# Kernel optimization log

Hardware: AMD Instinct MI355X
Metric: run time of the kernel (lower is better)

The kernel has to match this reference:

```python
import jax, jax.numpy as jnp
import numpy as np

EPS = 1e-6  # matches the ~1e-6 diagonal jitter added in tensor_log


def _make_spd(key, shape_bm, d):
    a = jax.random.normal(key, shape_bm + (d, d), dtype=jnp.float32)
    x = jnp.einsum('bmik,bmjk->bmij', a, a) / d
    return x + 0.1 * jnp.eye(d, dtype=jnp.float32)


def _make_stiefel(key, out_dim, in_dim):
    a = jax.random.normal(key, (in_dim, out_dim), dtype=jnp.float32)
    q, _ = jnp.linalg.qr(a)  # (in_dim, out_dim), orthonormal columns
    return q.T  # (out_dim, in_dim), semi-orthogonal rows


def setup_inputs() -> dict:
    key = jax.random.key(0)
    ks = jax.random.split(key, 8)
    bs, m, din, dqk, dv = 32, 64, 96, 48, 48
    return {
        'x1': _make_spd(ks[0], (bs, m), din),
        'x2': _make_spd(ks[1], (bs, m), din),
        'wq1': _make_stiefel(ks[2], dqk, din),
        'wk1': _make_stiefel(ks[3], dqk, din),
        'wv1': _make_stiefel(ks[4], dv, din),
        'wq2': _make_stiefel(ks[5], dqk, din),
        'wk2': _make_stiefel(ks[6], dqk, din),
        'wv2': _make_stiefel(ks[7], dv, din),
    }


def _logm(t):
    # symmetric matrix log via eigh (inputs SPD); tiny diag jitter as in torch tensor_log
    d = t.shape[-1]
    t = t + EPS * jnp.eye(d, dtype=t.dtype)
    s, u = jnp.linalg.eigh(t)
    return jnp.einsum('...ik,...k,...jk->...ij', u, jnp.log(s), u)


def _expm(t):
    s, u = jnp.linalg.eigh(t)
    return jnp.einsum('...ik,...k,...jk->...ij', u, jnp.exp(s), u)


def _bimap(x, w):
    # SPDTransform: W X W^T, W: (out, in), x: [..., in, in]
    return jnp.einsum('oi,...ij,pj->...op', w, x, w)


def reference(x1, x2, wq1, wk1, wv1, wq2, wk2, wv2):
    # per-stream q/k/v BiMap transforms, then concat along token axis
    Q = jnp.concatenate([_bimap(x1, wq1), _bimap(x2, wq2)], axis=1)  # [b, m, dqk, dqk]
    K = jnp.concatenate([_bimap(x1, wk1), _bimap(x2, wk2)], axis=1)
    V = jnp.concatenate([_bimap(x1, wv1), _bimap(x2, wv2)], axis=1)  # [b, m, dv, dv]

    logQ, logK, logV = _logm(Q), _logm(K), _logm(V)

    # log-Euclidean distance: sum of singular values of D D^T = ||D||_F^2,
    # D = logQ_j - logK_i. energy[b, i, j] matches torch repeat/expand layout
    q2 = jnp.sum(logQ * logQ, axis=(-2, -1))  # [b, m]
    k2 = jnp.sum(logK * logK, axis=(-2, -1))  # [b, m]
    cross = jnp.einsum('bjxy,bixy->bij', logQ, logK)  # [b, i(K), j(Q)]
    energy = q2[:, None, :] + k2[:, :, None] - 2.0 * cross
    energy = jnp.maximum(energy, 0.0)

    scores = 1.0 / (1.0 + jnp.log1p(energy))
    prob = jax.nn.softmax(scores, axis=-2)  # softmax over K index
    prob = jnp.transpose(prob, (0, 2, 1))   # [b, j, i]

    bs, m, dv, _ = V.shape
    mixed = (prob @ logV.reshape(bs, m, dv * dv)).reshape(bs, m, dv, dv)
    out = _expm(mixed)
    out = out[:, -1:, :, :]  # keep_only_last=True
    return out.reshape(-1, dv, dv)  # [bs, dv, dv]
```

## Files before the change

kernel.cpp:

```cpp
#include <hip/hip_runtime.h>
#include <math.h>

#define D_CHEB 24

typedef __attribute__((ext_vector_type(8))) short bf16x8;
typedef __attribute__((ext_vector_type(4))) short bf16x4;
typedef __attribute__((ext_vector_type(4))) float f32x4;
typedef __attribute__((ext_vector_type(4))) unsigned int u32x4;
typedef __attribute__((ext_vector_type(2))) unsigned int u32x2;

#if __has_builtin(__builtin_amdgcn_mfma_f32_16x16x16bf16_1k)
#define HAVE_MFMA16 1
#else
#define HAVE_MFMA16 0
#endif

struct Cheb {
    float c[D_CHEB + 1];
    float sm;
    float sbd;
};

__device__ __forceinline__ void split8(const f32x4 a, const f32x4 b,
                                       bf16x8& hi, bf16x8& lo)
{
    float v[8] = {a[0], a[1], a[2], a[3], b[0], b[1], b[2], b[3]};
    unsigned h16[8], l16[8];
    #pragma unroll
    for (int j = 0; j < 8; ++j) {
        unsigned u = __float_as_uint(v[j]);
        unsigned r = (u + 0x7FFFu + ((u >> 16) & 1u)) >> 16;
        h16[j] = r;
        float res = v[j] - __uint_as_float(r << 16);
        l16[j] = __float_as_uint(res) >> 16;
    }
    unsigned hw[4], lw[4];
    #pragma unroll
    for (int q = 0; q < 4; ++q) {
        hw[q] = h16[2 * q] | (h16[2 * q + 1] << 16);
        lw[q] = l16[2 * q] | (l16[2 * q + 1] << 16);
    }
    hi = __builtin_bit_cast(bf16x8, (u32x4){hw[0], hw[1], hw[2], hw[3]});
    lo = __builtin_bit_cast(bf16x8, (u32x4){lw[0], lw[1], lw[2], lw[3]});
}

__global__ __launch_bounds__(256) void split_w(
    const float* __restrict__ w0, const float* __restrict__ w1,
    const float* __restrict__ w2, const float* __restrict__ w3,
    const float* __restrict__ w4,
    unsigned short* __restrict__ whi, unsigned short* __restrict__ wlo)
{
    const float* W = (blockIdx.x == 0) ? w0 : (blockIdx.x == 1) ? w1
                   : (blockIdx.x == 2) ? w2 : (blockIdx.x == 3) ? w3 : w4;
    const int base = blockIdx.x * 4608;
    for (int e = threadIdx.x; e < 4608; e += 256) {
        float f = W[e];
        unsigned u = __float_as_uint(f);
        unsigned r = (u + 0x7FFFu + ((u >> 16) & 1u)) >> 16;
        whi[base + e] = (unsigned short)r;
        float res = f - __uint_as_float(r << 16);
        wlo[base + e] = (unsigned short)(__float_as_uint(res) >> 16);
    }
}

#define TLP 104
__global__ __launch_bounds__(64, 3) void bimap_kernel(
    const float* __restrict__ x1, const float* __restrict__ x2,
    const unsigned short* __restrict__ whi,
    const unsigned short* __restrict__ wlo,
    float* __restrict__ mats)
{
    __shared__ float Tlds[48 * TLP];
    const int bid = blockIdx.x, l = threadIdx.x;
    const int lc = l & 15, lg = l >> 4;

    const float* x; int wi[2]; size_t oo[2]; int npass;
    if (bid < 4096) {
        int b = bid >> 7, s = (bid >> 6) & 1, m = bid & 63;
        x = (s ? x2 : x1) + (size_t)(b * 64 + m) * 9216;
        wi[0] = s ? 2 : 0;
        wi[1] = s ? 3 : 1;
        oo[0] = (size_t)bid; oo[1] = (size_t)(4096 + bid); npass = 2;
    } else {
        int b = bid - 4096;
        x = x2 + (size_t)(b * 64 + 63) * 9216;
        wi[0] = 4; wi[1] = 4;
        oo[0] = (size_t)(8192 + b); oo[1] = oo[0]; npass = 1;
    }

    for (int pass = 0; pass < npass; ++pass) {
        const unsigned short* Wh = whi + wi[pass] * 4608;
        const unsigned short* Wl = wlo + wi[pass] * 4608;

        f32x4 C[3][6];
        #pragma unroll
        for (int tr = 0; tr < 3; ++tr)
            #pragma unroll
            for (int tc = 0; tc < 6; ++tc)
                C[tr][tc] = (f32x4){0.f, 0.f, 0.f, 0.f};
        #pragma unroll
        for (int kb = 0; kb < 3; ++kb) {
            bf16x8 ah[3], al[3];
            #pragma unroll
            for (int tr = 0; tr < 3; ++tr) {
                const int off = (16 * tr + lc) * 96 + kb * 32 + lg * 8;
                ah[tr] = *(const bf16x8*)(Wh + off);
                al[tr] = *(const bf16x8*)(Wl + off);
            }
            #pragma unroll
            for (int tc = 0; tc < 6; ++tc) {
                const float* xp = x + (16 * tc + lc) * 96 + kb * 32 + lg * 8;
                bf16x8 bh, bl;
                split8(*(const f32x4*)xp, *(const f32x4*)(xp + 4), bh, bl);
                #pragma unroll
                for (int tr = 0; tr < 3; ++tr) {
                    C[tr][tc] = __builtin_amdgcn_mfma_f32_16x16x32_bf16(ah[tr], bh, C[tr][tc], 0, 0, 0);
                    C[tr][tc] = __builtin_amdgcn_mfma_f32_16x16x32_bf16(ah[tr], bl, C[tr][tc], 0, 0, 0);
                    C[tr][tc] = __builtin_amdgcn_mfma_f32_16x16x32_bf16(al[tr], bh, C[tr][tc], 0, 0, 0);
                }
            }
        }
        #pragma unroll
        for (int tr = 0; tr < 3; ++tr)
            #pragma unroll
            for (int tc = 0; tc < 6; ++tc)
                #pragma unroll
                for (int q = 0; q < 4; ++q)
                    Tlds[(16 * tr + 4 * lg + q) * TLP + 16 * tc + lc] = C[tr][tc][q];

        f32x4 D[3][3];
        #pragma unroll
        for (int tr = 0; tr < 3; ++tr)
            #pragma unroll
            for (int tc = 0; tc < 3; ++tc)
                D[tr][tc] = (f32x4){0.f, 0.f, 0.f, 0.f};
        #pragma unroll
        for (int kb = 0; kb < 3; ++kb) {
            bf16x8 ah[3], al[3];
            #pragma unroll
            for (int tr = 0; tr < 3; ++tr) {
                const float* tp = &Tlds[(16 * tr + lc) * TLP + kb * 32 + lg * 8];
                split8(*(const f32x4*)tp, *(const f32x4*)(tp + 4), ah[tr], al[tr]);
            }
            #pragma unroll
            for (int tc = 0; tc < 3; ++tc) {
                const int off = (16 * tc + lc) * 96 + kb * 32 + lg * 8;
                bf16x8 bh = *(const bf16x8*)(Wh + off);
                bf16x8 bl = *(const bf16x8*)(Wl + off);
                #pragma unroll
                for (int tr = 0; tr < 3; ++tr) {
                    D[tr][tc] = __builtin_amdgcn_mfma_f32_16x16x32_bf16(ah[tr], bh, D[tr][tc], 0, 0, 0);
                    D[tr][tc] = __builtin_amdgcn_mfma_f32_16x16x32_bf16(ah[tr], bl, D[tr][tc], 0, 0, 0);
                    D[tr][tc] = __builtin_amdgcn_mfma_f32_16x16x32_bf16(al[tr], bh, D[tr][tc], 0, 0, 0);
                }
            }
        }
        float* out = mats + oo[pass] * 2304;
        #pragma unroll
        for (int tr = 0; tr < 3; ++tr)
            #pragma unroll
            for (int tc = 0; tc < 3; ++tc)
                #pragma unroll
                for (int q = 0; q < 4; ++q)
                    out[(16 * tr + 4 * lg + q) * 48 + 16 * tc + lc] = D[tr][tc][q];
    }
}

__global__ __launch_bounds__(64, 3) void logm_kernel(float* __restrict__ mats, Cheb co)
{
    __shared__ __align__(16) unsigned short Ybuf[2 * 48 * 64];
    char* ldsb = (char*)Ybuf;
    const int l = threadIdx.x;
    const int lc = l & 15, lg = l >> 4;
    const int rloc = lg * 4;
    float* A = mats + (size_t)blockIdx.x * 2304;

    bf16x8 Ah[3][2], Al[3][2];
    const float cD = co.c[D_CHEB], cD1 = co.c[D_CHEB - 1];
    #pragma unroll
    for (int tr = 0; tr < 3; ++tr) {
        #pragma unroll
        for (int kb = 0; kb < 2; ++kb) {
            const int row = 16 * tr + lc;
            const int k0 = kb * 32 + lg * 8;
            unsigned shw[4] = {0,0,0,0}, slw[4] = {0,0,0,0};
            unsigned yhw[4] = {0,0,0,0}, ylw[4] = {0,0,0,0};
            if (k0 < 48) {
                const float* ap = A + row * 48 + k0;
                f32x4 a0 = *(const f32x4*)ap;
                f32x4 a1 = *(const f32x4*)(ap + 4);
                float av[8] = {a0[0],a0[1],a0[2],a0[3],a1[0],a1[1],a1[2],a1[3]};
                unsigned sh[8], sl[8], yh[8], yl[8];
                #pragma unroll
                for (int j = 0; j < 8; ++j) {
                    const bool diag = (row == k0 + j);
                    float s = co.sm * av[j] + (diag ? co.sbd : 0.f);
                    float y = cD * s + (diag ? cD1 : 0.f);
                    unsigned us = __float_as_uint(s);
                    sh[j] = us >> 16;
                    sl[j] = __float_as_uint(s - __uint_as_float(us & 0xFFFF0000u)) >> 16;
                    unsigned uy = __float_as_uint(y);
                    yh[j] = uy >> 16;
                    yl[j] = __float_as_uint(y - __uint_as_float(uy & 0xFFFF0000u)) >> 16;
                }
                #pragma unroll
                for (int q = 0; q < 4; ++q) {
                    shw[q] = sh[2*q] | (sh[2*q+1] << 16);
                    slw[q] = sl[2*q] | (sl[2*q+1] << 16);
                    yhw[q] = yh[2*q] | (yh[2*q+1] << 16);
                    ylw[q] = yl[2*q] | (yl[2*q+1] << 16);
                }
            }
            Ah[tr][kb] = __builtin_bit_cast(bf16x8, (u32x4){shw[0],shw[1],shw[2],shw[3]});
            Al[tr][kb] = __builtin_bit_cast(bf16x8, (u32x4){slw[0],slw[1],slw[2],slw[3]});
            const int soff = row * 128 + ((2 * k0) ^ ((row & 7) << 4));
            *(u32x4*)(ldsb + soff)        = (u32x4){yhw[0],yhw[1],yhw[2],yhw[3]};
            *(u32x4*)(ldsb + 6144 + soff) = (u32x4){ylw[0],ylw[1],ylw[2],ylw[3]};
        }
    }

#if HAVE_MFMA16
    bf16x4 Ath[3], Atl[3];
    #pragma unroll
    for (int tr = 0; tr < 3; ++tr) {
        const int row = 16 * tr + lc;
        const int k0 = 32 + 4 * lg;
        f32x4 a = *(const f32x4*)(A + row * 48 + k0);
        unsigned sh[4], sl[4];
        #pragma unroll
        for (int j = 0; j < 4; ++j) {
            const bool diag = (row == k0 + j);
            float s = co.sm * a[j] + (diag ? co.sbd : 0.f);
            unsigned us = __float_as_uint(s);
            sh[j] = us >> 16;
            sl[j] = __float_as_uint(s - __uint_as_float(us & 0xFFFF0000u)) >> 16;
        }
        Ath[tr] = __builtin_bit_cast(bf16x4, (u32x2){sh[0] | (sh[1] << 16), sh[2] | (sh[3] << 16)});
        Atl[tr] = __builtin_bit_cast(bf16x4, (u32x2){sl[0] | (sl[1] << 16), sl[2] | (sl[3] << 16)});
    }
#endif

    f32x4 Ya[9], Yb[9];
    #pragma unroll
    for (int t = 0; t < 9; ++t) {
        const int tr = t / 3, tc = t % 3;
        #pragma unroll
        for (int q = 0; q < 4; ++q) {
            const int row = 16 * tr + rloc + q, col = 16 * tc + lc;
            const bool diag = (row == col);
            float a = A[row * 48 + col];
            float s = co.sm * a + (diag ? co.sbd : 0.f);
            Ya[t][q] = cD * s + (diag ? cD1 : 0.f);
            Yb[t][q] = diag ? cD : 0.f;
        }
    }

    int boff0[3];
    int bofft[3];
    int boff1[3];
    #pragma unroll
    for (int tc = 0; tc < 3; ++tc) {
        const int row = 16 * tc + lc;
        const int sw = (row & 7) << 4;
        boff0[tc] = row * 128 + ((lg * 16) ^ sw);
        bofft[tc] = row * 128 + ((64 + lg * 8) ^ sw);
        boff1[tc] = row * 128 + ((64 + lg * 16) ^ sw);
    }
    int woffT[9];
    #pragma unroll
    for (int t = 0; t < 9; ++t) {
        const int tr = t / 3, tc = t % 3;
        const int row = 16 * tc + lc;
        woffT[t] = row * 128 + (((32 * tr + 8 * lg)) ^ ((row & 7) << 4));
    }

    auto MM = [&](f32x4 (&T)[9]) {
        #pragma unroll
        for (int tc = 0; tc < 3; ++tc) {
            {
                bf16x8 bh = *(const bf16x8*)(ldsb + boff0[tc]);
                bf16x8 bl = *(const bf16x8*)(ldsb + 6144 + boff0[tc]);
                #pragma unroll
                for (int tr = 0; tr < 3; ++tr)
                    T[tr*3+tc] = __builtin_amdgcn_mfma_f32_16x16x32_bf16(Ah[tr][0], bh, T[tr*3+tc], 0, 0, 0);
                #pragma unroll
                for (int tr = 0; tr < 3; ++tr)
                    T[tr*3+tc] = __builtin_amdgcn_mfma_f32_16x16x32_bf16(Ah[tr][0], bl, T[tr*3+tc], 0, 0, 0);
                #pragma unroll
                for (int tr = 0; tr < 3; ++tr)
                    T[tr*3+tc] = __builtin_amdgcn_mfma_f32_16x16x32_bf16(Al[tr][0], bh, T[tr*3+tc], 0, 0, 0);
            }
#if HAVE_MFMA16
            {
                bf16x4 bh = *(const bf16x4*)(ldsb + bofft[tc]);
                bf16x4 bl = *(const bf16x4*)(ldsb + 6144 + bofft[tc]);
                #pragma unroll
                for (int tr = 0; tr < 3; ++tr)
                    T[tr*3+tc] = __builtin_amdgcn_mfma_f32_16x16x16bf16_1k(Ath[tr], bh, T[tr*3+tc], 0, 0, 0);
                #pragma unroll
                for (int tr = 0; tr < 3; ++tr)
                    T[tr*3+tc] = __builtin_amdgcn_mfma_f32_16x16x16bf16_1k(Ath[tr], bl, T[tr*3+tc], 0, 0, 0);
                #pragma unroll
                for (int tr = 0; tr < 3; ++tr)
                    T[tr*3+tc] = __builtin_amdgcn_mfma_f32_16x16x16bf16_1k(Atl[tr], bh, T[tr*3+tc], 0, 0, 0);
            }
#else
            {
                bf16x8 bh = *(const bf16x8*)(ldsb + boff1[tc]);
                bf16x8 bl = *(const bf16x8*)(ldsb + 6144 + boff1[tc]);
                #pragma unroll
                for (int tr = 0; tr < 3; ++tr)
                    T[tr*3+tc] = __builtin_amdgcn_mfma_f32_16x16x32_bf16(Ah[tr][1], bh, T[tr*3+tc], 0, 0, 0);
                #pragma unroll
                for (int tr = 0; tr < 3; ++tr)
                    T[tr*3+tc] = __builtin_amdgcn_mfma_f32_16x16x32_bf16(Ah[tr][1], bl, T[tr*3+tc], 0, 0, 0);
                #pragma unroll
                for (int tr = 0; tr < 3; ++tr)
                    T[tr*3+tc] = __builtin_amdgcn_mfma_f32_16x16x32_bf16(Al[tr][1], bh, T[tr*3+tc], 0, 0, 0);
            }
#endif
        }
    };
    auto SPLITWT = [&](f32x4 (&T)[9]) {
        #pragma unroll
        for (int t = 0; t < 9; ++t) {
            unsigned u0 = __float_as_uint(T[t][0]);
            unsigned u1 = __float_as_uint(T[t][1]);
            unsigned u2 = __float_as_uint(T[t][2]);
            unsigned u3 = __float_as_uint(T[t][3]);
            unsigned h01 = (u1 & 0xFFFF0000u) | (u0 >> 16);
            unsigned h23 = (u3 & 0xFFFF0000u) | (u2 >> 16);
            float r0 = T[t][0] - __uint_as_float(u0 & 0xFFFF0000u);
            float r1 = T[t][1] - __uint_as_float(u1 & 0xFFFF0000u);
            float r2 = T[t][2] - __uint_as_float(u2 & 0xFFFF0000u);
            float r3 = T[t][3] - __uint_as_float(u3 & 0xFFFF0000u);
            unsigned l01 = (__float_as_uint(r1) & 0xFFFF0000u) | (__float_as_uint(r0) >> 16);
            unsigned l23 = (__float_as_uint(r3) & 0xFFFF0000u) | (__float_as_uint(r2) >> 16);
            const int off = woffT[t];
            *(u32x2*)(ldsb + off)        = (u32x2){h01, h23};
            *(u32x2*)(ldsb + 6144 + off) = (u32x2){l01, l23};
        }
    };
    auto INITK = [&](f32x4 (&T)[9], float ck) {
        #pragma unroll
        for (int t = 0; t < 9; ++t) {
            const int tr = t / 3, tc = t % 3;
            #pragma unroll
            for (int q = 0; q < 4; ++q) {
                const float d = (tr == tc && rloc + q == lc) ? ck : 0.f;
                T[t][q] = d - T[t][q];
            }
        }
    };

    for (int k = D_CHEB - 2; k >= 2; k -= 2) {
        INITK(Yb, co.c[k]);     MM(Yb);  SPLITWT(Yb);
        INITK(Ya, co.c[k - 1]); MM(Ya);  SPLITWT(Ya);
    }
    #pragma unroll
    for (int t = 0; t < 9; ++t) {
        const int tr = t / 3, tc = t % 3;
        #pragma unroll
        for (int q = 0; q < 4; ++q) {
            const float d = (tr == tc && rloc + q == lc) ? co.c[0] : 0.f;
            Yb[t][q] = d - 2.f * Yb[t][q];
        }
    }
    MM(Yb);
    #pragma unroll
    for (int t = 0; t < 9; ++t) {
        const int tr = t / 3, tc = t % 3;
        #pragma unroll
        for (int q = 0; q < 4; ++q)
            A[(16 * tr + rloc + q) * 48 + 16 * tc + lc] = Yb[t][q];
    }
}

__global__ __launch_bounds__(64) void energy_kernel(const float* __restrict__ mats,
                                                    float* __restrict__ sc)
{
    const int i = blockIdx.x, b = blockIdx.y, lane = threadIdx.x;
    const float* K = mats + (size_t)(b * 128 + i) * 2304;
    const float* Q = mats + (size_t)(8192 + b) * 2304;
    float p = 0.f;
    #pragma unroll
    for (int j = 0; j < 9; ++j) {
        int f = (lane + 64 * j) * 4;
        float4 kv = *(const float4*)(K + f);
        float4 qv = *(const float4*)(Q + f);
        float dx = kv.x - qv.x, dy = kv.y - qv.y, dz = kv.z - qv.z, dw = kv.w - qv.w;
        p += dx * dx + dy * dy + dz * dz + dw * dw;
    }
    #pragma unroll
    for (int off = 32; off >= 1; off >>= 1) p += __shfl_xor(p, off, 64);
    if (lane == 0)
        sc[b * 128 + i] = 1.f / (1.f + log1pf(fmaxf(p, 0.f)));
}

__global__ __launch_bounds__(64) void softmax_kernel(float* __restrict__ sc)
{
    const int b = blockIdx.x, lane = threadIdx.x;
    float s0 = sc[b * 128 + lane], s1 = sc[b * 128 + 64 + lane];
    float m = fmaxf(s0, s1);
    #pragma unroll
    for (int off = 32; off >= 1; off >>= 1) m = fmaxf(m, __shfl_xor(m, off, 64));
    float e0 = expf(s0 - m), e1 = expf(s1 - m);
    float sum = e0 + e1;
    #pragma unroll
    for (int off = 32; off >= 1; off >>= 1) sum += __shfl_xor(sum, off, 64);
    sc[b * 128 + lane] = e0 / sum;
    sc[b * 128 + 64 + lane] = e1 / sum;
}

__global__ __launch_bounds__(256) void mix_kernel(const float* __restrict__ mats,
                                                  const float* __restrict__ sc,
                                                  float* __restrict__ mixed)
{
    __shared__ float w[128];
    const int b = blockIdx.y, g = blockIdx.x, tid = threadIdx.x;
    if (tid < 128) w[tid] = sc[b * 128 + tid];
    __syncthreads();
    const int e = g * 256 + tid;
    float acc = 0.f;
    for (int i = 0; i < 128; ++i)
        acc += w[i] * mats[(size_t)(4096 + b * 128 + i) * 2304 + e];
    mixed[(size_t)b * 2304 + e] = acc;
}

__global__ __launch_bounds__(256) void expm_kernel(const float* __restrict__ mixed,
                                                   float* __restrict__ out)
{
    __shared__ float Bs[48][49];
    __shared__ float Ra[48][49];
    __shared__ float Rb[48][49];
    const int b = blockIdx.x, tid = threadIdx.x;
    const float* M = mixed + (size_t)b * 2304;
    for (int e = tid; e < 2304; e += 256) {
        int r = e / 48, c = e % 48;
        float v = 0.25f * M[e];
        Bs[r][c] = v;
        Ra[r][c] = ((r == c) ? 1.f : 0.f) + v * (1.f / 12.f);
    }
    __syncthreads();
    const int tr = tid >> 4, tc = tid & 15;
    const int r0 = tr * 3, c0 = tc * 3;
    float* cur = &Ra[0][0];
    float* nxt = &Rb[0][0];
    for (int k = 11; k >= 1; --k) {
        const float invk = 1.f / (float)k;
        float acc[3][3];
        #pragma unroll
        for (int i = 0; i < 3; ++i)
            #pragma unroll
            for (int j = 0; j < 3; ++j) acc[i][j] = 0.f;
        #pragma unroll 4
        for (int kk = 0; kk < 48; ++kk) {
            float a0 = Bs[r0][kk], a1 = Bs[r0 + 1][kk], a2 = Bs[r0 + 2][kk];
            float b0 = cur[kk * 49 + c0], b1 = cur[kk * 49 + c0 + 1], b2 = cur[kk * 49 + c0 + 2];
            acc[0][0] += a0 * b0; acc[0][1] += a0 * b1; acc[0][2] += a0 * b2;
            acc[1][0] += a1 * b0; acc[1][1] += a1 * b1; acc[1][2] += a1 * b2;
            acc[2][0] += a2 * b0; acc[2][1] += a2 * b1; acc[2][2] += a2 * b2;
        }
        #pragma unroll
        for (int i = 0; i < 3; ++i)
            #pragma unroll
            for (int j = 0; j < 3; ++j)
                nxt[(r0 + i) * 49 + (c0 + j)] =
                    ((r0 + i) == (c0 + j) ? 1.f : 0.f) + acc[i][j] * invk;
        __syncthreads();
        float* t = cur; cur = nxt; nxt = t;
    }
    for (int sq = 0; sq < 2; ++sq) {
        float acc[3][3];
        #pragma unroll
        for (int i = 0; i < 3; ++i)
            #pragma unroll
            for (int j = 0; j < 3; ++j) acc[i][j] = 0.f;
        #pragma unroll 4
        for (int kk = 0; kk < 48; ++kk) {
            float a0 = cur[(r0) * 49 + kk], a1 = cur[(r0 + 1) * 49 + kk], a2 = cur[(r0 + 2) * 49 + kk];
            float b0 = cur[kk * 49 + c0], b1 = cur[kk * 49 + c0 + 1], b2 = cur[kk * 49 + c0 + 2];
            acc[0][0] += a0 * b0; acc[0][1] += a0 * b1; acc[0][2] += a0 * b2;
            acc[1][0] += a1 * b0; acc[1][1] += a1 * b1; acc[1][2] += a1 * b2;
            acc[2][0] += a2 * b0; acc[2][1] += a2 * b1; acc[2][2] += a2 * b2;
        }
        __syncthreads();
        #pragma unroll
        for (int i = 0; i < 3; ++i)
            #pragma unroll
            for (int j = 0; j < 3; ++j) nxt[(r0 + i) * 49 + (c0 + j)] = acc[i][j];
        __syncthreads();
        float* t = cur; cur = nxt; nxt = t;
    }
    #pragma unroll
    for (int i = 0; i < 3; ++i)
        #pragma unroll
        for (int j = 0; j < 3; ++j)
            out[(size_t)b * 2304 + (r0 + i) * 48 + (c0 + j)] = cur[(r0 + i) * 49 + (c0 + j)];
}

extern "C" void kernel_launch(void* const* d_in, const int* in_sizes, int n_in,
                              void* d_out, int out_size, void* d_ws, size_t ws_size,
                              hipStream_t stream)
{
    (void)in_sizes; (void)n_in; (void)out_size; (void)ws_size;
    const float* x1  = (const float*)d_in[0];
    const float* x2  = (const float*)d_in[1];
    const float* wk1 = (const float*)d_in[3];
    const float* wv1 = (const float*)d_in[4];
    const float* wq2 = (const float*)d_in[5];
    const float* wk2 = (const float*)d_in[6];
    const float* wv2 = (const float*)d_in[7];
    float* mats  = (float*)d_ws;
    float* mixed = mats + (size_t)8224 * 2304;
    float* scbuf = mixed + (size_t)32 * 2304;
    unsigned short* whi = (unsigned short*)(scbuf + 4096);
    unsigned short* wlo = whi + 5 * 4608;
    float* out   = (float*)d_out;

    Cheb co;
    {
        const double a = 0.098, bb = 5.5;
        const int N = 256;
        for (int k = 0; k <= D_CHEB; ++k) {
            double sacc = 0.0;
            for (int j = 0; j < N; ++j) {
                double th = M_PI * (j + 0.5) / N;
                double xj = 0.5 * (a + bb) + 0.5 * (bb - a) * cos(th);
                sacc += log(xj) * cos(k * th);
            }
            double ck = 2.0 * sacc / N;
            if (k == 0) ck *= 0.5;
            if (k >= 1) ck *= 0.5;
            co.c[k] = (float)ck;
        }
        co.sm  = (float)(4.0 / (bb - a));
        co.sbd = (float)((4.0 * 1e-6 - 2.0 * (a + bb)) / (bb - a));
    }

    split_w<<<5, 256, 0, stream>>>(wk1, wv1, wk2, wv2, wq2, whi, wlo);
    bimap_kernel<<<4128, 64, 0, stream>>>(x1, x2, whi, wlo, mats);
    logm_kernel<<<8224, 64, 0, stream>>>(mats, co);
    energy_kernel<<<dim3(128, 32), 64, 0, stream>>>(mats, scbuf);
    softmax_kernel<<<32, 64, 0, stream>>>(scbuf);
    mix_kernel<<<dim3(9, 32), 256, 0, stream>>>(mats, scbuf, mixed);
    expm_kernel<<<32, 256, 0, stream>>>(mixed, out);
}
```

Baseline: 415.2 us.

## Split logm Chebyshev evaluation across three column-strip blocks per matrix

The logm kernel now launches a 2D grid in which each of three blocks per matrix computes one 16-column strip of the Chebyshev polynomial. The full A operand stays in registers while only one strip of Y goes to LDS. Because the column strips of the recurrence are independent, this is meant to cut per-block register and LDS use, raise occupancy and shorten each wave's serial MFMA chain. The cost is loading and splitting A three times per matrix, and each wave having fewer independent accumulators to hide MFMA latency.

```diff
diff --git a/kernel.cpp b/kernel.cpp
--- a/kernel.cpp
+++ b/kernel.cpp
@@ -166,14 +166,15 @@
     }
 }
 
-__global__ __launch_bounds__(64, 3) void logm_kernel(float* __restrict__ mats, Cheb co)
-{
-    __shared__ __align__(16) unsigned short Ybuf[2 * 48 * 64];
+__global__ __launch_bounds__(64, 4) void logm_kernel(float* __restrict__ mats, Cheb co)
+{
+    __shared__ __align__(16) unsigned short Ybuf[2 * 16 * 64];
     char* ldsb = (char*)Ybuf;
     const int l = threadIdx.x;
     const int lc = l & 15, lg = l >> 4;
     const int rloc = lg * 4;
-    float* A = mats + (size_t)blockIdx.x * 2304;
+    const int w = blockIdx.x;
+    float* A = mats + (size_t)blockIdx.y * 2304;
 
     bf16x8 Ah[3][2], Al[3][2];
     const float cD = co.c[D_CHEB], cD1 = co.c[D_CHEB - 1];
@@ -213,9 +214,11 @@
             }
             Ah[tr][kb] = __builtin_bit_cast(bf16x8, (u32x4){shw[0],shw[1],shw[2],shw[3]});
             Al[tr][kb] = __builtin_bit_cast(bf16x8, (u32x4){slw[0],slw[1],slw[2],slw[3]});
-            const int soff = row * 128 + ((2 * k0) ^ ((row & 7) << 4));
-            *(u32x4*)(ldsb + soff)        = (u32x4){yhw[0],yhw[1],yhw[2],yhw[3]};
-            *(u32x4*)(ldsb + 6144 + soff) = (u32x4){ylw[0],ylw[1],ylw[2],ylw[3]};
+            if (tr == w) {
+                const int soff = lc * 128 + ((2 * k0) ^ ((lc & 7) << 4));
+                *(u32x4*)(ldsb + soff)        = (u32x4){yhw[0],yhw[1],yhw[2],yhw[3]};
+                *(u32x4*)(ldsb + 2048 + soff) = (u32x4){ylw[0],ylw[1],ylw[2],ylw[3]};
+            }
         }
     }
 
@@ -240,13 +243,17 @@
     }
 #endif
 
-    f32x4 Ya[9], Yb[9];
-    #pragma unroll
-    for (int t = 0; t < 9; ++t) {
-        const int tr = t / 3, tc = t % 3;
+    float dm[4];
+    #pragma unroll
+    for (int q = 0; q < 4; ++q) dm[q] = (rloc + q == lc) ? 1.f : 0.f;
+
+    f32x4 Ya[3], Yb[3];
+    #pragma unroll
+    for (int t = 0; t < 3; ++t) {
+        const int col = 16 * w + lc;
         #pragma unroll
         for (int q = 0; q < 4; ++q) {
-            const int row = 16 * tr + rloc + q, col = 16 * tc + lc;
+            const int row = 16 * t + rloc + q;
             const bool diag = (row == col);
             float a = A[row * 48 + col];
             float s = co.sm * a + (diag ? co.sbd : 0.f);
@@ -255,75 +262,62 @@
         }
     }
 
-    int boff0[3];
-    int bofft[3];
-    int boff1[3];
-    #pragma unroll
-    for (int tc = 0; tc < 3; ++tc) {
-        const int row = 16 * tc + lc;
-        const int sw = (row & 7) << 4;
-        boff0[tc] = row * 128 + ((lg * 16) ^ sw);
-        bofft[tc] = row * 128 + ((64 + lg * 8) ^ sw);
-        boff1[tc] = row * 128 + ((64 + lg * 16) ^ sw);
-    }
-    int woffT[9];
-    #pragma unroll
-    for (int t = 0; t < 9; ++t) {
-        const int tr = t / 3, tc = t % 3;
-        const int row = 16 * tc + lc;
-        woffT[t] = row * 128 + (((32 * tr + 8 * lg)) ^ ((row & 7) << 4));
-    }
-
-    auto MM = [&](f32x4 (&T)[9]) {
-        #pragma unroll
-        for (int tc = 0; tc < 3; ++tc) {
-            {
-                bf16x8 bh = *(const bf16x8*)(ldsb + boff0[tc]);
-                bf16x8 bl = *(const bf16x8*)(ldsb + 6144 + boff0[tc]);
-                #pragma unroll
-                for (int tr = 0; tr < 3; ++tr)
-                    T[tr*3+tc] = __builtin_amdgcn_mfma_f32_16x16x32_bf16(Ah[tr][0], bh, T[tr*3+tc], 0, 0, 0);
-                #pragma unroll
-                for (int tr = 0; tr < 3; ++tr)
-                    T[tr*3+tc] = __builtin_amdgcn_mfma_f32_16x16x32_bf16(Ah[tr][0], bl, T[tr*3+tc], 0, 0, 0);
-                #pragma unroll
-                for (int tr = 0; tr < 3; ++tr)
-                    T[tr*3+tc] = __builtin_amdgcn_mfma_f32_16x16x32_bf16(Al[tr][0], bh, T[tr*3+tc], 0, 0, 0);
-            }
+    const int sw = (lc & 7) << 4;
+    const int boff0 = lc * 128 + ((16 * lg) ^ sw);
+    const int bofft = lc * 128 + ((64 + 8 * lg) ^ sw);
+    const int boff1 = lc * 128 + ((64 + 16 * lg) ^ sw);
+    int woffT[3];
+    #pragma unroll
+    for (int tr = 0; tr < 3; ++tr)
+        woffT[tr] = lc * 128 + ((32 * tr + 8 * lg) ^ sw);
+
+    auto MM = [&](f32x4 (&T)[3]) {
+        {
+            bf16x8 bh = *(const bf16x8*)(ldsb + boff0);
+            bf16x8 bl = *(const bf16x8*)(ldsb + 2048 + boff0);
+            #pragma unroll
+            for (int tr = 0; tr < 3; ++tr)
+                T[tr] = __builtin_amdgcn_mfma_f32_16x16x32_bf16(Ah[tr][0], bh, T[tr], 0, 0, 0);
+            #pragma unroll
+            for (int tr = 0; tr < 3; ++tr)
+                T[tr] = __builtin_amdgcn_mfma_f32_16x16x32_bf16(Ah[tr][0], bl, T[tr], 0, 0, 0);
+            #pragma unroll
+            for (int tr = 0; tr < 3; ++tr)
+                T[tr] = __builtin_amdgcn_mfma_f32_16x16x32_bf16(Al[tr][0], bh, T[tr], 0, 0, 0);
+        }
 #if HAVE_MFMA16
-            {
-                bf16x4 bh = *(const bf16x4*)(ldsb + bofft[tc]);
-                bf16x4 bl = *(const bf16x4*)(ldsb + 6144 + bofft[tc]);
-                #pragma unroll
-                for (int tr = 0; tr < 3; ++tr)
-                    T[tr*3+tc] = __builtin_amdgcn_mfma_f32_16x16x16bf16_1k(Ath[tr], bh, T[tr*3+tc], 0, 0, 0);
-                #pragma unroll
-                for (int tr = 0; tr < 3; ++tr)
-                    T[tr*3+tc] = __builtin_amdgcn_mfma_f32_16x16x16bf16_1k(Ath[tr], bl, T[tr*3+tc], 0, 0, 0);
-                #pragma unroll
-                for (int tr = 0; tr < 3; ++tr)
-                    T[tr*3+tc] = __builtin_amdgcn_mfma_f32_16x16x16bf16_1k(Atl[tr], bh, T[tr*3+tc], 0, 0, 0);
-            }
+        {
+            bf16x4 bh = *(const bf16x4*)(ldsb + bofft);
+            bf16x4 bl = *(const bf16x4*)(ldsb + 2048 + bofft);
+            #pragma unroll
+            for (int tr = 0; tr < 3; ++tr)
+                T[tr] = __builtin_amdgcn_mfma_f32_16x16x16bf16_1k(Ath[tr], bh, T[tr], 0, 0, 0);
+            #pragma unroll
+            for (int tr = 0; tr < 3; ++tr)
+                T[tr] = __builtin_amdgcn_mfma_f32_16x16x16bf16_1k(Ath[tr], bl, T[tr], 0, 0, 0);
+            #pragma unroll
+            for (int tr = 0; tr < 3; ++tr)
+                T[tr] = __builtin_amdgcn_mfma_f32_16x16x16bf16_1k(Atl[tr], bh, T[tr], 0, 0, 0);
+        }
 #else
-            {
-                bf16x8 bh = *(const bf16x8*)(ldsb + boff1[tc]);
-                bf16x8 bl = *(const bf16x8*)(ldsb + 6144 + boff1[tc]);
-                #pragma unroll
-                for (int tr = 0; tr < 3; ++tr)
-                    T[tr*3+tc] = __builtin_amdgcn_mfma_f32_16x16x32_bf16(Ah[tr][1], bh, T[tr*3+tc], 0, 0, 0);
-                #pragma unroll
-                for (int tr = 0; tr < 3; ++tr)
-                    T[tr*3+tc] = __builtin_amdgcn_mfma_f32_16x16x32_bf16(Ah[tr][1], bl, T[tr*3+tc], 0, 0, 0);
-                #pragma unroll
-                for (int tr = 0; tr < 3; ++tr)
-                    T[tr*3+tc] = __builtin_amdgcn_mfma_f32_16x16x32_bf16(Al[tr][1], bh, T[tr*3+tc], 0, 0, 0);
-            }
+        {
+            bf16x8 bh = *(const bf16x8*)(ldsb + boff1);
+            bf16x8 bl = *(const bf16x8*)(ldsb + 2048 + boff1);
+            #pragma unroll
+            for (int tr = 0; tr < 3; ++tr)
+                T[tr] = __builtin_amdgcn_mfma_f32_16x16x32_bf16(Ah[tr][1], bh, T[tr], 0, 0, 0);
+            #pragma unroll
+            for (int tr = 0; tr < 3; ++tr)
+                T[tr] = __builtin_amdgcn_mfma_f32_16x16x32_bf16(Ah[tr][1], bl, T[tr], 0, 0, 0);
+            #pragma unroll
+            for (int tr = 0; tr < 3; ++tr)
+                T[tr] = __builtin_amdgcn_mfma_f32_16x16x32_bf16(Al[tr][1], bh, T[tr], 0, 0, 0);
+        }
 #endif
-        }
     };
-    auto SPLITWT = [&](f32x4 (&T)[9]) {
-        #pragma unroll
-        for (int t = 0; t < 9; ++t) {
+    auto SPLITWT = [&](f32x4 (&T)[3]) {
+        #pragma unroll
+        for (int t = 0; t < 3; ++t) {
             unsigned u0 = __float_as_uint(T[t][0]);
             unsigned u1 = __float_as_uint(T[t][1]);
             unsigned u2 = __float_as_uint(T[t][2]);
@@ -338,18 +332,16 @@
             unsigned l23 = (__float_as_uint(r3) & 0xFFFF0000u) | (__float_as_uint(r2) >> 16);
             const int off = woffT[t];
             *(u32x2*)(ldsb + off)        = (u32x2){h01, h23};
-            *(u32x2*)(ldsb + 6144 + off) = (u32x2){l01, l23};
+            *(u32x2*)(ldsb + 2048 + off) = (u32x2){l01, l23};
         }
     };
-    auto INITK = [&](f32x4 (&T)[9], float ck) {
-        #pragma unroll
-        for (int t = 0; t < 9; ++t) {
-            const int tr = t / 3, tc = t % 3;
-            #pragma unroll
-            for (int q = 0; q < 4; ++q) {
-                const float d = (tr == tc && rloc + q == lc) ? ck : 0.f;
-                T[t][q] = d - T[t][q];
-            }
+    auto INITK = [&](f32x4 (&T)[3], float ck) {
+        #pragma unroll
+        for (int t = 0; t < 3; ++t) {
+            const float cw = (t == w) ? ck : 0.f;
+            #pragma unroll
+            for (int q = 0; q < 4; ++q)
+                T[t][q] = fmaf(cw, dm[q], -T[t][q]);
         }
     };
 
@@ -357,23 +349,22 @@
         INITK(Yb, co.c[k]);     MM(Yb);  SPLITWT(Yb);
         INITK(Ya, co.c[k - 1]); MM(Ya);  SPLITWT(Ya);
     }
-    #pragma unroll
-    for (int t = 0; t < 9; ++t) {
-        const int tr = t / 3, tc = t % 3;
-        #pragma unroll
-        for (int q = 0; q < 4; ++q) {
-            const float d = (tr == tc && rloc + q == lc) ? co.c[0] : 0.f;
-            Yb[t][q] = d - 2.f * Yb[t][q];
+    {
+        const float c0w = (w >= 0) ? co.c[0] : 0.f;
+        #pragma unroll
+        for (int t = 0; t < 3; ++t) {
+            const float cw = (t == w) ? c0w : 0.f;
+            #pragma unroll
+            for (int q = 0; q < 4; ++q)
+                Yb[t][q] = fmaf(-2.f, Yb[t][q], cw * dm[q]);
         }
     }
     MM(Yb);
     #pragma unroll
-    for (int t = 0; t < 9; ++t) {
-        const int tr = t / 3, tc = t % 3;
+    for (int t = 0; t < 3; ++t)
         #pragma unroll
         for (int q = 0; q < 4; ++q)
-            A[(16 * tr + rloc + q) * 48 + 16 * tc + lc] = Yb[t][q];
-    }
+            A[(16 * t + rloc + q) * 48 + 16 * w + lc] = Yb[t][q];
 }
 
 __global__ __launch_bounds__(64) void energy_kernel(const float* __restrict__ mats,
@@ -540,7 +531,7 @@
 
     split_w<<<5, 256, 0, stream>>>(wk1, wv1, wk2, wv2, wq2, whi, wlo);
     bimap_kernel<<<4128, 64, 0, stream>>>(x1, x2, whi, wlo, mats);
-    logm_kernel<<<8224, 64, 0, stream>>>(mats, co);
+    logm_kernel<<<dim3(3, 8224), 64, 0, stream>>>(mats, co);
     energy_kernel<<<dim3(128, 32), 64, 0, stream>>>(mats, scbuf);
     softmax_kernel<<<32, 64, 0, stream>>>(scbuf);
     mix_kernel<<<dim3(9, 32), 256, 0, stream>>>(mats, scbuf, mixed);
```

Result: no change. 423.2 us (+1.9%).
